# Performance work log

Measured on AMD Instinct MI355X. Metric: run time of the kernel, lower is better.

The kernel has to match this reference:

```python
import jax, jax.numpy as jnp
import numpy as np
from itertools import product

DIM = 384
HEADS = 8
DIM_HEAD = 64
INNER = HEADS * DIM_HEAD  # 512
KS = 3                    # kernel_size (attention window)
PAD = KS // 2
W_WIN = KS * KS           # 9
SCALE = DIM_HEAD ** -0.5


def setup_inputs() -> dict:
    key = jax.random.key(0)
    k1, k2, k3, k4, k5 = jax.random.split(key, 5)
    B, H, W = 4, 56, 56
    x = jax.random.normal(k1, (B, DIM, H, W), dtype=jnp.float32)
    # 1x1 conv weights stored as (out_ch, in_ch)
    Wq = jax.random.normal(k2, (INNER, DIM), dtype=jnp.float32) * (DIM ** -0.5)
    Wkv = jax.random.normal(k3, (2 * INNER, DIM), dtype=jnp.float32) * (DIM ** -0.5)
    Wo = jax.random.normal(k4, (DIM, INNER), dtype=jnp.float32) * (INNER ** -0.5)
    bo = jax.random.normal(k5, (DIM,), dtype=jnp.float32) * 0.01
    return {"x": x, "Wq": Wq, "Wkv": Wkv, "Wo": Wo, "bo": bo}


def _conv1x1(x, w):
    # x: (B,Cin,H,W), w: (Cout,Cin) -> (B,Cout,H,W)
    return jnp.einsum('bchw,oc->bohw', x, w)


def reference(x, Wq, Wkv, Wo, bo):
    B, C, H, W = x.shape
    q = _conv1x1(x, Wq)                       # (B, INNER, H, W)
    kv = _conv1x1(x, Wkv)                     # (B, 2*INNER, H, W)
    k, v = jnp.split(kv, 2, axis=1)
    # split channels heads-major, matching torch reshape (B, heads, dh, H, W)
    q = q.reshape(B, HEADS, DIM_HEAD, H, W)
    k = k.reshape(B, HEADS, DIM_HEAD, H, W)
    v = v.reshape(B, HEADS, DIM_HEAD, H, W)
    # zero-pad spatial dims (matches F.unfold zero padding: padded taps get logit 0)
    k_pad = jnp.pad(k, ((0, 0), (0, 0), (0, 0), (PAD, PAD), (PAD, PAD)))
    v_pad = jnp.pad(v, ((0, 0), (0, 0), (0, 0), (PAD, PAD), (PAD, PAD)))
    offsets = list(product(range(KS), range(KS)))  # row-major = unfold order
    # dots: (B, heads, H, W, w)
    dots = jnp.stack([
        jnp.einsum('bhdxy,bhdxy->bhxy', q, k_pad[:, :, :, i:i + H, j:j + W])
        for (i, j) in offsets
    ], axis=-1) * SCALE
    attn = jax.nn.softmax(dots, axis=-1)      # softmax over the 9-tap window
    # weighted sum of shifted v: (B, heads, dh, H, W)
    out = sum(
        attn[:, :, None, :, :, w_idx] * v_pad[:, :, :, i:i + H, j:j + W]
        for w_idx, (i, j) in enumerate(offsets)
    )
    out = out.reshape(B, INNER, H, W)
    return _conv1x1(out, Wo) + bo[None, :, None, None]
```

## Files before the change

kernel.cpp:

```cpp
#include <hip/hip_runtime.h>


#define HW 3136
#define WIMG 56
#define QKV_CH 1536
#define SCALE 0.125f
#define KSTR 72
#define NROWS 242
#define QKV_T 6422528

typedef __bf16 bf16x8_t __attribute__((ext_vector_type(8)));
typedef float f32x4_t __attribute__((ext_vector_type(4)));
typedef unsigned short ushort8 __attribute__((ext_vector_type(8)));

__device__ __forceinline__ float bf2f(unsigned short u) {
    return __uint_as_float(((unsigned int)u) << 16);
}
__device__ __forceinline__ unsigned short f2bf(float f) {
    unsigned int u = __float_as_uint(f);
    u += 0x7FFFu + ((u >> 16) & 1u);
    return (unsigned short)(u >> 16);
}

__device__ __forceinline__ void gll16(const unsigned short* g, unsigned short* l) {
    __builtin_amdgcn_global_load_lds(
        (const __attribute__((address_space(1))) unsigned int*)g,
        (__attribute__((address_space(3))) unsigned int*)l,
        16, 0, 0);
}

__global__ __launch_bounds__(256) void cvt_all(
    const float* __restrict__ x,
    const float* __restrict__ Wq, const float* __restrict__ Wkv,
    const float* __restrict__ Wo,
    unsigned short* __restrict__ xT,
    unsigned short* __restrict__ wT, unsigned short* __restrict__ wT3)
{
    __shared__ unsigned short Tl[64 * 36];
    const int bx = blockIdx.x;
    const int t = threadIdx.x;

    if (bx < 2400) {
        const int sblk = bx % 50;
        const int kblk = (bx / 50) % 12;
        const int b    = bx / 600;

        if (sblk == 49) {
            unsigned short* dst = xT + (((size_t)b * 25 + 24) * 12 + kblk) * 4096 + 2048;
            *reinterpret_cast<uint4*>(dst + t * 8) = (uint4){0, 0, 0, 0};
            return;
        }

        const float* xp = x + ((size_t)b * 384 + (size_t)kblk * 32) * HW + sblk * 64;
        const int c = t >> 3;
#pragma unroll
        for (int i = 0; i < 2; i++) {
            const int sc = (t & 7) + 8 * i;
            const float4 v = *reinterpret_cast<const float4*>(xp + (size_t)c * HW + sc * 4);
            const int s4 = sc * 4;
            Tl[(s4 + 0) * 36 + c] = f2bf(v.x);
            Tl[(s4 + 1) * 36 + c] = f2bf(v.y);
            Tl[(s4 + 2) * 36 + c] = f2bf(v.z);
            Tl[(s4 + 3) * 36 + c] = f2bf(v.w);
        }
        __syncthreads();

        const int row = t >> 2, gran = t & 3;
        const uint2 lo = *reinterpret_cast<const uint2*>(&Tl[row * 36 + gran * 8]);
        const uint2 hi = *reinterpret_cast<const uint2*>(&Tl[row * 36 + gran * 8 + 4]);
        uint4 o; o.x = lo.x; o.y = lo.y; o.z = hi.x; o.w = hi.y;
        unsigned short* dst = xT + (((size_t)b * 25 + (sblk >> 1)) * 12 + kblk) * 4096
                            + (sblk & 1) * 2048;
        *reinterpret_cast<uint4*>(dst + t * 8) = o;
        return;
    }

    const int i = (bx - 2400) * 256 + t;
    if (i < 73728) {
        const int g = i & 3;
        const int idx3 = i >> 2;
        const int o128 = idx3 & 127;
        const int rest = idx3 >> 7;
        const int kb = rest % 12, oblk = rest / 12;
        const int o = oblk * 128 + o128;
        const int k0 = kb * 32 + g * 8;
        const float* src = (o < 512) ? (Wq + (size_t)o * 384 + k0)
                                     : (Wkv + (size_t)(o - 512) * 384 + k0);
        const float4 v0 = *reinterpret_cast<const float4*>(src);
        const float4 v1 = *reinterpret_cast<const float4*>(src + 4);
        uint4 u;
        u.x = (unsigned int)f2bf(v0.x) | ((unsigned int)f2bf(v0.y) << 16);
        u.y = (unsigned int)f2bf(v0.z) | ((unsigned int)f2bf(v0.w) << 16);
        u.z = (unsigned int)f2bf(v1.x) | ((unsigned int)f2bf(v1.y) << 16);
        u.w = (unsigned int)f2bf(v1.z) | ((unsigned int)f2bf(v1.w) << 16);
        reinterpret_cast<uint4*>(wT)[i] = u;
    } else {
        const int j = i - 73728;
        const int g = j & 3;
        const int idx3 = j >> 2;
        const int o128 = idx3 & 127;
        const int rest = idx3 >> 7;
        const int kb = rest % 16, oblk = rest / 16;
        const int o = oblk * 128 + o128;
        const float* src = Wo + (size_t)o * 512 + kb * 32 + g * 8;
        const float4 v0 = *reinterpret_cast<const float4*>(src);
        const float4 v1 = *reinterpret_cast<const float4*>(src + 4);
        uint4 u;
        u.x = (unsigned int)f2bf(v0.x) | ((unsigned int)f2bf(v0.y) << 16);
        u.y = (unsigned int)f2bf(v0.z) | ((unsigned int)f2bf(v0.w) << 16);
        u.z = (unsigned int)f2bf(v1.x) | ((unsigned int)f2bf(v1.y) << 16);
        u.w = (unsigned int)f2bf(v1.z) | ((unsigned int)f2bf(v1.w) << 16);
        reinterpret_cast<uint4*>(wT3)[j] = u;
    }
}

__global__ __launch_bounds__(256) void gemm1(
    const unsigned short* __restrict__ xT,
    const unsigned short* __restrict__ wT,
    unsigned short* __restrict__ qkvT)
{
    __shared__ __align__(16) unsigned short A_lds[2][128 * 32];
    __shared__ __align__(16) unsigned short B_lds[2][128 * 32];

    const int lin = blockIdx.x;
    const int swz = (lin & 7) * 150 + (lin >> 3);
    const int sblk = swz % 25;
    const int oblk = (swz / 25) % 12;
    const int b    = swz / 300;

    const int t  = threadIdx.x;
    const int lane = t & 63, w = t >> 6;
    const int quad = lane >> 4, mrow = lane & 15;
    const int wm = w >> 1, wn = w & 1;

    const unsigned short* wsrc = wT + ((size_t)oblk * 12) * 4096;
    const unsigned short* xsrc = xT + (((size_t)b * 25 + sblk) * 12) * 4096;

    f32x4_t acc[4][4];
#pragma unroll
    for (int m = 0; m < 4; m++)
#pragma unroll
        for (int n = 0; n < 4; n++) acc[m][n] = (f32x4_t){0.f, 0.f, 0.f, 0.f};

    for (int kb = 0; kb < 6; kb++) {
        const size_t k0 = (size_t)(2 * kb) * 4096;
        const size_t k1 = (size_t)(2 * kb + 1) * 4096;
        __syncthreads();
        gll16(wsrc + k0 + t * 8,        A_lds[0] + t * 8);
        gll16(wsrc + k0 + 2048 + t * 8, A_lds[0] + 2048 + t * 8);
        gll16(wsrc + k1 + t * 8,        A_lds[1] + t * 8);
        gll16(wsrc + k1 + 2048 + t * 8, A_lds[1] + 2048 + t * 8);
        gll16(xsrc + k0 + t * 8,        B_lds[0] + t * 8);
        gll16(xsrc + k0 + 2048 + t * 8, B_lds[0] + 2048 + t * 8);
        gll16(xsrc + k1 + t * 8,        B_lds[1] + t * 8);
        gll16(xsrc + k1 + 2048 + t * 8, B_lds[1] + 2048 + t * 8);
        __syncthreads();

#pragma unroll
        for (int ks = 0; ks < 2; ks++) {
            bf16x8_t af[4], bfr[4];
#pragma unroll
            for (int m = 0; m < 4; m++)
                af[m] = *reinterpret_cast<const bf16x8_t*>(&A_lds[ks][(wm * 64 + m * 16 + mrow) * 32 + quad * 8]);
#pragma unroll
            for (int n = 0; n < 4; n++)
                bfr[n] = *reinterpret_cast<const bf16x8_t*>(&B_lds[ks][(wn * 64 + n * 16 + mrow) * 32 + quad * 8]);
#pragma unroll
            for (int m = 0; m < 4; m++)
#pragma unroll
                for (int n = 0; n < 4; n++)
                    acc[m][n] = __builtin_amdgcn_mfma_f32_16x16x32_bf16(af[m], bfr[n], acc[m][n], 0, 0, 0);
        }
    }

    const int which = oblk >> 2;
    const int hq = (oblk & 3) * 2 + wm;
    const int s0 = sblk * 128 + wn * 64;
    unsigned short* outb = qkvT + (size_t)which * QKV_T
                         + ((size_t)(b * 8 + hq) * HW) * 64;
#pragma unroll
    for (int m = 0; m < 4; m++) {
        const int d0 = m * 16 + quad * 4;
#pragma unroll
        for (int n = 0; n < 4; n++) {
            const int ss = s0 + n * 16 + mrow;
            if (ss < HW) {
                uint2 u;
                u.x = (unsigned int)f2bf(acc[m][n][0]) | ((unsigned int)f2bf(acc[m][n][1]) << 16);
                u.y = (unsigned int)f2bf(acc[m][n][2]) | ((unsigned int)f2bf(acc[m][n][3]) << 16);
                *reinterpret_cast<uint2*>(outb + (size_t)ss * 64 + d0) = u;
            }
        }
    }
}

__global__ __launch_bounds__(256) void natt2(
    const unsigned short* __restrict__ qkvT,
    unsigned short* __restrict__ aoT)
{
    __shared__ __align__(16) unsigned short KV[NROWS * KSTR];
    __shared__ float dred[9 * 2 * 128];

    const int lin = blockIdx.x;
    const int swz = (lin & 7) * 100 + (lin >> 3);
    const int sblk = swz % 25;
    const int h = (swz / 25) & 7;
    const int b = swz / 200;

    const int t = threadIdx.x;
    const int p  = t & 127;
    const int dq = t >> 7;
    const int s0 = sblk * 128;
    const int s  = s0 + p;
    const int sc = min(s, HW - 1);
    const int y  = sc / WIMG, xx = sc % WIMG;

    const unsigned short* qg = qkvT + ((size_t)(b * 8 + h) * HW) * 64;
    const unsigned short* kg = qg + (size_t)QKV_T;
    const unsigned short* vg = qg + (size_t)(2 * QKV_T);

#pragma unroll
    for (int i = 0; i < 8; i++) {
        const int f = i * 256 + t;
        if (f < NROWS * 8) {
            const int row = f >> 3, c8 = f & 7;
            int srow = s0 - 57 + row;
            srow = min(max(srow, 0), HW - 1);
            const uint4 k4 = *reinterpret_cast<const uint4*>(kg + (size_t)srow * 64 + c8 * 8);
            *reinterpret_cast<uint4*>(&KV[row * KSTR + c8 * 8]) = k4;
        }
    }

    int   roff[9];
    float msk[9];
#pragma unroll
    for (int ty = 0; ty < 3; ty++)
#pragma unroll
        for (int tx = 0; tx < 3; tx++) {
            const int tap = ty * 3 + tx;
            const int ny = y + ty - 1, nx = xx + tx - 1;
            const bool v = (ny >= 0) && (ny < WIMG) && (nx >= 0) && (nx < WIMG);
            roff[tap] = (v ? ((ty - 1) * WIMG + (tx - 1)) : 0) * KSTR;
            msk[tap]  = v ? 1.f : 0.f;
        }

    float qv[32];
#pragma unroll
    for (int c = 0; c < 4; c++) {
        const uint4 q4 = *reinterpret_cast<const uint4*>(qg + (size_t)sc * 64 + dq * 32 + c * 8);
        qv[c*8+0] = bf2f((unsigned short)(q4.x & 0xffff)); qv[c*8+1] = bf2f((unsigned short)(q4.x >> 16));
        qv[c*8+2] = bf2f((unsigned short)(q4.y & 0xffff)); qv[c*8+3] = bf2f((unsigned short)(q4.y >> 16));
        qv[c*8+4] = bf2f((unsigned short)(q4.z & 0xffff)); qv[c*8+5] = bf2f((unsigned short)(q4.z >> 16));
        qv[c*8+6] = bf2f((unsigned short)(q4.w & 0xffff)); qv[c*8+7] = bf2f((unsigned short)(q4.w >> 16));
    }

    __syncthreads();

    const int rbase = (57 + p) * KSTR + dq * 32;

    float dots[9];
#pragma unroll
    for (int tp = 0; tp < 9; tp++) dots[tp] = 0.f;
#pragma unroll
    for (int ch = 0; ch < 4; ch++) {
#pragma unroll
        for (int tp = 0; tp < 9; tp++) {
            const ushort8 kk = *reinterpret_cast<const ushort8*>(&KV[rbase + roff[tp] + ch * 8]);
#pragma unroll
            for (int j = 0; j < 8; j++)
                dots[tp] += qv[ch * 8 + j] * bf2f(kk[j]);
        }
    }

    __syncthreads();

#pragma unroll
    for (int tp = 0; tp < 9; tp++) dred[(tp * 2 + dq) * 128 + p] = dots[tp];
#pragma unroll
    for (int i = 0; i < 8; i++) {
        const int f = i * 256 + t;
        if (f < NROWS * 8) {
            const int row = f >> 3, c8 = f & 7;
            int srow = s0 - 57 + row;
            srow = min(max(srow, 0), HW - 1);
            const uint4 v4 = *reinterpret_cast<const uint4*>(vg + (size_t)srow * 64 + c8 * 8);
            *reinterpret_cast<uint4*>(&KV[row * KSTR + c8 * 8]) = v4;
        }
    }

    __syncthreads();

    float mx = -1e30f, dt[9];
#pragma unroll
    for (int tp = 0; tp < 9; tp++) {
        const float sum = dred[(tp * 2 + 0) * 128 + p] + dred[(tp * 2 + 1) * 128 + p];
        dt[tp] = msk[tp] * (sum * SCALE);
        mx = fmaxf(mx, dt[tp]);
    }
    float se = 0.f, w9[9];
#pragma unroll
    for (int tp = 0; tp < 9; tp++) { w9[tp] = __expf(dt[tp] - mx); se += w9[tp]; }
    const float inv = 1.f / se;
#pragma unroll
    for (int tp = 0; tp < 9; tp++) w9[tp] *= inv * msk[tp];

    float o[32];
#pragma unroll
    for (int dd = 0; dd < 32; dd++) o[dd] = 0.f;
#pragma unroll
    for (int ch = 0; ch < 4; ch++) {
        ushort8 vfr[9];
#pragma unroll
        for (int tp = 0; tp < 9; tp++)
            vfr[tp] = *reinterpret_cast<const ushort8*>(&KV[rbase + roff[tp] + ch * 8]);
#pragma unroll
        for (int j = 0; j < 8; j++)
#pragma unroll
            for (int tp = 0; tp < 9; tp++)
                o[ch * 8 + j] += w9[tp] * bf2f(vfr[tp][j]);
    }

    if (s < HW) {
        __align__(16) unsigned short ov[32];
#pragma unroll
        for (int dd = 0; dd < 32; dd++) ov[dd] = f2bf(o[dd]);
        unsigned short* dst = aoT + (((size_t)(b * 49 + (s >> 6))) * 16 + (h * 2 + dq)) * 2048
                            + (s & 63) * 32;
        *reinterpret_cast<uint4*>(dst)      = *reinterpret_cast<const uint4*>(ov);
        *reinterpret_cast<uint4*>(dst + 8)  = *reinterpret_cast<const uint4*>(ov + 8);
        *reinterpret_cast<uint4*>(dst + 16) = *reinterpret_cast<const uint4*>(ov + 16);
        *reinterpret_cast<uint4*>(dst + 24) = *reinterpret_cast<const uint4*>(ov + 24);
    }
}

__global__ __launch_bounds__(256) void gemm3(
    const unsigned short* __restrict__ aoT,
    const unsigned short* __restrict__ wT3,
    const float* __restrict__ bias,
    float* __restrict__ out)
{
    __shared__ __align__(16) unsigned short A_lds[2][128 * 32];
    __shared__ __align__(16) unsigned short B_lds[2][64 * 32];

    const int sblk = blockIdx.x;
    const int oblk = blockIdx.y;
    const int b  = blockIdx.z;
    const int t  = threadIdx.x;
    const int lane = t & 63, w = t >> 6;
    const int quad = lane >> 4, mrow = lane & 15;
    const int wm = w >> 1, wn = w & 1;

    const unsigned short* asrc = wT3 + (size_t)oblk * 16 * 4096;
    const unsigned short* bsrc = aoT + ((size_t)(b * 49 + sblk)) * 16 * 2048;

    f32x4_t acc[4][2];
#pragma unroll
    for (int m = 0; m < 4; m++)
#pragma unroll
        for (int n = 0; n < 2; n++) acc[m][n] = (f32x4_t){0.f, 0.f, 0.f, 0.f};

    for (int kb = 0; kb < 8; kb++) {
        const size_t a0 = (size_t)(2 * kb) * 4096;
        const size_t a1 = (size_t)(2 * kb + 1) * 4096;
        const size_t b0 = (size_t)(2 * kb) * 2048;
        const size_t b1 = (size_t)(2 * kb + 1) * 2048;
        __syncthreads();
        gll16(asrc + a0 + t * 8,        A_lds[0] + t * 8);
        gll16(asrc + a0 + 2048 + t * 8, A_lds[0] + 2048 + t * 8);
        gll16(asrc + a1 + t * 8,        A_lds[1] + t * 8);
        gll16(asrc + a1 + 2048 + t * 8, A_lds[1] + 2048 + t * 8);
        gll16(bsrc + b0 + t * 8,        B_lds[0] + t * 8);
        gll16(bsrc + b1 + t * 8,        B_lds[1] + t * 8);
        __syncthreads();

#pragma unroll
        for (int ks = 0; ks < 2; ks++) {
            bf16x8_t af[4], bfr[2];
#pragma unroll
            for (int m = 0; m < 4; m++)
                af[m] = *reinterpret_cast<const bf16x8_t*>(&A_lds[ks][(wm * 64 + m * 16 + mrow) * 32 + quad * 8]);
#pragma unroll
            for (int n = 0; n < 2; n++)
                bfr[n] = *reinterpret_cast<const bf16x8_t*>(&B_lds[ks][(wn * 32 + n * 16 + mrow) * 32 + quad * 8]);
#pragma unroll
            for (int m = 0; m < 4; m++)
#pragma unroll
                for (int n = 0; n < 2; n++)
                    acc[m][n] = __builtin_amdgcn_mfma_f32_16x16x32_bf16(af[m], bfr[n], acc[m][n], 0, 0, 0);
        }
    }

    const int o0 = oblk * 128 + wm * 64;
    const int s0 = sblk * 64 + wn * 32;
    float* outb = out + (size_t)b * 384 * HW;
#pragma unroll
    for (int m = 0; m < 4; m++)
#pragma unroll
        for (int n = 0; n < 2; n++) {
            const int ss = s0 + n * 16 + mrow;
#pragma unroll
            for (int r = 0; r < 4; r++) {
                const int oo = o0 + m * 16 + quad * 4 + r;
                outb[(size_t)oo * HW + ss] = acc[m][n][r] + bias[oo];
            }
        }
}

extern "C" void kernel_launch(void* const* d_in, const int* in_sizes, int n_in,
                              void* d_out, int out_size, void* d_ws, size_t ws_size,
                              hipStream_t stream) {
    const float* x   = (const float*)d_in[0];
    const float* Wq  = (const float*)d_in[1];
    const float* Wkv = (const float*)d_in[2];
    const float* Wo  = (const float*)d_in[3];
    const float* bo  = (const float*)d_in[4];
    float* out = (float*)d_out;

    unsigned short* xT   = (unsigned short*)d_ws;
    unsigned short* wT   = xT + (size_t)4915200;
    unsigned short* wT3  = wT + (size_t)589824;
    unsigned short* qkvT = wT3 + (size_t)196608;
    unsigned short* aoT  = qkvT + (size_t)(3 * QKV_T);

    cvt_all<<<dim3(2784), 256, 0, stream>>>(x, Wq, Wkv, Wo, xT, wT, wT3);

    gemm1<<<dim3(1200), 256, 0, stream>>>(xT, wT, qkvT);
    natt2<<<dim3(800), 256, 0, stream>>>(qkvT, aoT);
    gemm3<<<dim3(49, 3, 4), 256, 0, stream>>>(aoT, wT3, bo, out);
}
```

Baseline: 135.0 us.

## Give each attention thread a full head dim, drop the reduction, and remap gemm3 blocks

The neighborhood-attention kernel now has each thread handle one pixel across all 64 head channels over a 256-pixel tile. This removes the cross-thread dot reduction through shared memory and one barrier's worth of traffic, and the halo overhead per pixel shrinks. The cost is higher register pressure (64 q and 64 output floats), possibly lower occupancy, and fewer blocks (416 instead of 800). The output-projection GEMM launch is flattened to 1D with an XCD-aware block remap so that blocks sharing the same activations land on the same die.

```diff
diff --git a/kernel.cpp b/kernel.cpp
--- a/kernel.cpp
+++ b/kernel.cpp
@@ -6,7 +6,7 @@
 #define QKV_CH 1536
 #define SCALE 0.125f
 #define KSTR 72
-#define NROWS 242
+#define NROWS2 370
 #define QKV_T 6422528
 
 typedef __bf16 bf16x8_t __attribute__((ext_vector_type(8)));
@@ -198,20 +198,17 @@
     const unsigned short* __restrict__ qkvT,
     unsigned short* __restrict__ aoT)
 {
-    __shared__ __align__(16) unsigned short KV[NROWS * KSTR];
-    __shared__ float dred[9 * 2 * 128];
+    __shared__ __align__(16) unsigned short KV[NROWS2 * KSTR];
 
     const int lin = blockIdx.x;
-    const int swz = (lin & 7) * 100 + (lin >> 3);
-    const int sblk = swz % 25;
-    const int h = (swz / 25) & 7;
-    const int b = swz / 200;
+    const int swz = (lin & 7) * 52 + (lin >> 3);
+    const int sblk = swz % 13;
+    const int h = (swz / 13) & 7;
+    const int b = swz / 104;
 
     const int t = threadIdx.x;
-    const int p  = t & 127;
-    const int dq = t >> 7;
-    const int s0 = sblk * 128;
-    const int s  = s0 + p;
+    const int s0 = sblk * 256;
+    const int s  = s0 + t;
     const int sc = min(s, HW - 1);
     const int y  = sc / WIMG, xx = sc % WIMG;
 
@@ -220,9 +217,9 @@
     const unsigned short* vg = qg + (size_t)(2 * QKV_T);
 
 #pragma unroll
-    for (int i = 0; i < 8; i++) {
+    for (int i = 0; i < 12; i++) {
         const int f = i * 256 + t;
-        if (f < NROWS * 8) {
+        if (f < NROWS2 * 8) {
             const int row = f >> 3, c8 = f & 7;
             int srow = s0 - 57 + row;
             srow = min(max(srow, 0), HW - 1);
@@ -244,10 +241,10 @@
             msk[tap]  = v ? 1.f : 0.f;
         }
 
-    float qv[32];
-#pragma unroll
-    for (int c = 0; c < 4; c++) {
-        const uint4 q4 = *reinterpret_cast<const uint4*>(qg + (size_t)sc * 64 + dq * 32 + c * 8);
+    float qv[64];
+#pragma unroll
+    for (int c = 0; c < 8; c++) {
+        const uint4 q4 = *reinterpret_cast<const uint4*>(qg + (size_t)sc * 64 + c * 8);
         qv[c*8+0] = bf2f((unsigned short)(q4.x & 0xffff)); qv[c*8+1] = bf2f((unsigned short)(q4.x >> 16));
         qv[c*8+2] = bf2f((unsigned short)(q4.y & 0xffff)); qv[c*8+3] = bf2f((unsigned short)(q4.y >> 16));
         qv[c*8+4] = bf2f((unsigned short)(q4.z & 0xffff)); qv[c*8+5] = bf2f((unsigned short)(q4.z >> 16));
@@ -256,13 +253,13 @@
 
     __syncthreads();
 
-    const int rbase = (57 + p) * KSTR + dq * 32;
+    const int rbase = (57 + t) * KSTR;
 
     float dots[9];
 #pragma unroll
     for (int tp = 0; tp < 9; tp++) dots[tp] = 0.f;
 #pragma unroll
-    for (int ch = 0; ch < 4; ch++) {
+    for (int ch = 0; ch < 8; ch++) {
 #pragma unroll
         for (int tp = 0; tp < 9; tp++) {
             const ushort8 kk = *reinterpret_cast<const ushort8*>(&KV[rbase + roff[tp] + ch * 8]);
@@ -275,11 +272,9 @@
     __syncthreads();
 
 #pragma unroll
-    for (int tp = 0; tp < 9; tp++) dred[(tp * 2 + dq) * 128 + p] = dots[tp];
-#pragma unroll
-    for (int i = 0; i < 8; i++) {
+    for (int i = 0; i < 12; i++) {
         const int f = i * 256 + t;
-        if (f < NROWS * 8) {
+        if (f < NROWS2 * 8) {
             const int row = f >> 3, c8 = f & 7;
             int srow = s0 - 57 + row;
             srow = min(max(srow, 0), HW - 1);
@@ -293,8 +288,7 @@
     float mx = -1e30f, dt[9];
 #pragma unroll
     for (int tp = 0; tp < 9; tp++) {
-        const float sum = dred[(tp * 2 + 0) * 128 + p] + dred[(tp * 2 + 1) * 128 + p];
-        dt[tp] = msk[tp] * (sum * SCALE);
+        dt[tp] = msk[tp] * (dots[tp] * SCALE);
         mx = fmaxf(mx, dt[tp]);
     }
     float se = 0.f, w9[9];
@@ -304,11 +298,11 @@
 #pragma unroll
     for (int tp = 0; tp < 9; tp++) w9[tp] *= inv * msk[tp];
 
-    float o[32];
-#pragma unroll
-    for (int dd = 0; dd < 32; dd++) o[dd] = 0.f;
-#pragma unroll
-    for (int ch = 0; ch < 4; ch++) {
+    float o[64];
+#pragma unroll
+    for (int dd = 0; dd < 64; dd++) o[dd] = 0.f;
+#pragma unroll
+    for (int ch = 0; ch < 8; ch++) {
         ushort8 vfr[9];
 #pragma unroll
         for (int tp = 0; tp < 9; tp++)
@@ -321,15 +315,17 @@
     }
 
     if (s < HW) {
-        __align__(16) unsigned short ov[32];
-#pragma unroll
-        for (int dd = 0; dd < 32; dd++) ov[dd] = f2bf(o[dd]);
-        unsigned short* dst = aoT + (((size_t)(b * 49 + (s >> 6))) * 16 + (h * 2 + dq)) * 2048
-                            + (s & 63) * 32;
-        *reinterpret_cast<uint4*>(dst)      = *reinterpret_cast<const uint4*>(ov);
-        *reinterpret_cast<uint4*>(dst + 8)  = *reinterpret_cast<const uint4*>(ov + 8);
-        *reinterpret_cast<uint4*>(dst + 16) = *reinterpret_cast<const uint4*>(ov + 16);
-        *reinterpret_cast<uint4*>(dst + 24) = *reinterpret_cast<const uint4*>(ov + 24);
+        __align__(16) unsigned short ov[64];
+#pragma unroll
+        for (int dd = 0; dd < 64; dd++) ov[dd] = f2bf(o[dd]);
+        unsigned short* dst0 = aoT + (((size_t)(b * 49 + (s >> 6))) * 16 + (h * 2)) * 2048
+                             + (s & 63) * 32;
+        unsigned short* dst1 = dst0 + 2048;
+#pragma unroll
+        for (int c = 0; c < 4; c++) {
+            *reinterpret_cast<uint4*>(dst0 + c * 8) = *reinterpret_cast<const uint4*>(ov + c * 8);
+            *reinterpret_cast<uint4*>(dst1 + c * 8) = *reinterpret_cast<const uint4*>(ov + 32 + c * 8);
+        }
     }
 }
 
@@ -342,9 +338,13 @@
     __shared__ __align__(16) unsigned short A_lds[2][128 * 32];
     __shared__ __align__(16) unsigned short B_lds[2][64 * 32];
 
-    const int sblk = blockIdx.x;
-    const int oblk = blockIdx.y;
-    const int b  = blockIdx.z;
+    const int lin = blockIdx.x;
+    const int xcd = lin & 7, idx = lin >> 3;
+    const int wid = (xcd < 4) ? (xcd * 74 + idx) : (296 + (xcd - 4) * 73 + idx);
+    const int oblk = wid % 3;
+    const int sblk = (wid / 3) % 49;
+    const int b    = wid / 147;
+
     const int t  = threadIdx.x;
     const int lane = t & 63, w = t >> 6;
     const int quad = lane >> 4, mrow = lane & 15;
@@ -425,6 +425,6 @@
     cvt_all<<<dim3(2784), 256, 0, stream>>>(x, Wq, Wkv, Wo, xT, wT, wT3);
 
     gemm1<<<dim3(1200), 256, 0, stream>>>(xT, wT, qkvT);
-    natt2<<<dim3(800), 256, 0, stream>>>(qkvT, aoT);
-    gemm3<<<dim3(49, 3, 4), 256, 0, stream>>>(aoT, wT3, bo, out);
-}
+    natt2<<<dim3(416), 256, 0, stream>>>(qkvT, aoT);
+    gemm3<<<dim3(588), 256, 0, stream>>>(aoT, wT3, bo, out);
+}
```

Measured after the change: 140.6 us. +4.2%, slower.
